# Optimization experiments

Measured on AMD Instinct MI355X. Metric: run time of the kernel, lower is better.

Reference implementation:

```python
import jax, jax.numpy as jnp
import numpy as np

B, T, W, R, N = 32, 256, 128, 4, 128
IFACE = R * W + 3 * W + 5 * R + 3   # 919
INSZ = (R + 1) * W                  # 640
DELTA = 1e-6

def _lstm_step(x, h, c, Wih, Whh, bih, bhh):
    g = x @ Wih.T + bih + h @ Whh.T + bhh
    i, f, gg, o = jnp.split(g, 4, axis=-1)
    c = jax.nn.sigmoid(f) * c + jax.nn.sigmoid(i) * jnp.tanh(gg)
    return jax.nn.sigmoid(o) * jnp.tanh(c), c

def _cosine(mem, keys):
    # mem [b,n,w], keys [b,h,w] -> [b,h,n]
    mn = mem / (jnp.linalg.norm(mem, axis=2, keepdims=True) + DELTA)
    kn = keys / (jnp.linalg.norm(keys, axis=2, keepdims=True) + DELTA)
    return jnp.einsum('bhw,bnw->bhn', kn, mn)

def _memory_step(xi, st):
    # xi: [b, IFACE] interface vector; st: DNC memory state
    mem, link, prec, rw, ww, usage = st
    b = xi.shape[0]
    o1 = R * W; o2 = o1 + R; o3 = o2 + W; o4 = o3 + 1
    o5 = o4 + W; o6 = o5 + W; o7 = o6 + R; o8 = o7 + 1; o9 = o8 + 1
    read_keys = jnp.tanh(xi[:, :o1].reshape(b, R, W))
    read_str = jax.nn.softplus(xi[:, o1:o2])
    write_key = jnp.tanh(xi[:, o2:o3])
    write_str = jax.nn.softplus(xi[:, o3:o4])
    erase = jax.nn.sigmoid(xi[:, o4:o5])
    write_vec = jnp.tanh(xi[:, o5:o6])
    free_gates = jax.nn.sigmoid(xi[:, o6:o7])
    alloc_gate = jax.nn.sigmoid(xi[:, o7:o8])
    write_gate = jax.nn.sigmoid(xi[:, o8:o9])
    read_modes = jax.nn.softmax(xi[:, o9:].reshape(b, R, 3), axis=-1)
    # usage vector update (single write head)
    usage = usage + (1 - usage) * ww
    usage = usage * jnp.prod(1 - free_gates[:, :, None] * rw, axis=1)
    # write content weighting [b,n]
    wc = jax.nn.softmax(_cosine(mem, write_key[:, None, :])[:, 0, :] * write_str, axis=1)
    # allocation weighting: sort ascending, exclusive cumprod, unsort
    u = DELTA + (1 - DELTA) * usage
    phi = jnp.argsort(u, axis=1)
    su = jnp.take_along_axis(u, phi, axis=1)
    prod_su = jnp.cumprod(jnp.concatenate([jnp.ones((b, 1), u.dtype), su], axis=1), axis=1)[:, :-1]
    alloc = jnp.take_along_axis((1 - su) * prod_su, jnp.argsort(phi, axis=1), axis=1)
    # write weighting [b,n]
    ww = write_gate * (alloc_gate * alloc + (1 - alloc_gate) * wc)
    # erase then write
    mem = mem * (1 - ww[:, :, None] * erase[:, None, :]) + ww[:, :, None] * write_vec[:, None, :]
    # temporal link matrix [b,n,n], zero diagonal
    link = (1 - ww[:, :, None] - ww[:, None, :]) * link + ww[:, :, None] * prec[:, None, :]
    link = link * (1 - jnp.eye(N, dtype=link.dtype))
    prec = (1 - jnp.sum(ww, axis=1, keepdims=True)) * prec + ww
    # read weighting: content + forward/backward temporal modes
    rc = jax.nn.softmax(_cosine(mem, read_keys) * read_str[:, :, None], axis=2)
    fw = jnp.einsum('bij,brj->bri', link, rw)
    bw = jnp.einsum('brj,bji->bri', rw, link)
    rw = read_modes[:, :, 0:1] * bw + read_modes[:, :, 1:2] * fw + read_modes[:, :, 2:3] * rc
    read_vecs = jnp.einsum('brn,bnw->bwr', rw, mem)  # [b,w,r] as used by controller
    return read_vecs, (mem, link, prec, rw, ww, usage)

def _forward(input, enc_Wih, enc_Whh, enc_bih, enc_bhh, ctl_Wih, ctl_Whh, ctl_bih, ctl_bhh, iface_W, iface_b, out_W, out_b):
    dt = input.dtype
    h0 = jnp.zeros((B, W), dt)
    def enc_step(carry, x_t):
        h, c = _lstm_step(x_t, carry[0], carry[1], enc_Wih, enc_Whh, enc_bih, enc_bhh)
        return (h, c), h
    _, enc = jax.lax.scan(enc_step, (h0, h0), jnp.swapaxes(input, 0, 1))  # enc: [T,B,W]
    z = lambda *s: jnp.zeros(s, dt)
    mem0 = (z(B, N, W), z(B, N, N), z(B, N), z(B, R, N), z(B, N), z(B, N))
    def step(carry, enc_t):
        h, c, rv, mst = carry
        # cat([b,w,1],[b,w,r]) then flatten -> interleaved per memory-cell element, as in torch
        x = jnp.concatenate([enc_t[:, :, None], rv], axis=2).reshape(B, INSZ)
        h, c = _lstm_step(x, h, c, ctl_Wih, ctl_Whh, ctl_bih, ctl_bhh)
        xi = h @ iface_W.T + iface_b
        rv, mst = _memory_step(xi, mst)
        out_t = jnp.concatenate([h, rv.reshape(B, W * R)], axis=1) @ out_W.T + out_b
        return (h, c, rv, mst), out_t
    _, outs = jax.lax.scan(step, (h0, h0, z(B, W, R), mem0), enc)
    return jnp.swapaxes(outs, 0, 1)  # [B,T,W]

def setup_inputs():
    key = jax.random.key(0)
    ks = jax.random.split(key, 8)
    p = lambda k, s: jax.random.normal(k, s, jnp.float32) * 0.05
    return {
        'input': jax.random.normal(ks[0], (B, T, W), jnp.float32),
        'source_lengths': jnp.full((B,), T, jnp.int32),
        'enc_Wih': p(ks[1], (4 * W, W)), 'enc_Whh': p(ks[2], (4 * W, W)),
        'enc_bih': jnp.zeros((4 * W,), jnp.float32), 'enc_bhh': jnp.zeros((4 * W,), jnp.float32),
        'ctl_Wih': p(ks[3], (4 * W, INSZ)), 'ctl_Whh': p(ks[4], (4 * W, W)),
        'ctl_bih': jnp.zeros((4 * W,), jnp.float32), 'ctl_bhh': jnp.zeros((4 * W,), jnp.float32),
        'iface_W': p(ks[5], (IFACE, W)), 'iface_b': jnp.zeros((IFACE,), jnp.float32),
        'out_W': p(ks[6], (W, INSZ)), 'out_b': jnp.zeros((W,), jnp.float32),
    }

def reference(input, source_lengths, enc_Wih, enc_Whh, enc_bih, enc_bhh, ctl_Wih, ctl_Whh, ctl_bih, ctl_bhh, iface_W, iface_b, out_W, out_b):
    # source_lengths are all == T (full-length sequences), so pack/pad is identity.
    return _forward(input, enc_Wih, enc_Whh, enc_bih, enc_bhh, ctl_Wih, ctl_Whh, ctl_bih, ctl_bhh, iface_W, iface_b, out_W, out_b)
```

## Files before the change

kernel.cpp:

```cpp
#include <hip/hip_runtime.h>

typedef unsigned short u16;
typedef unsigned int u32;

#define NT 1024
#define Bv 32
#define Tv 256
#define Wv 128
#define Rv 4
#define Nv 128
#define DELTAv 1e-6f

__device__ __forceinline__ float bf2f(u16 u){
  union { u32 i; float f; } c; c.i = ((u32)u) << 16; return c.f;
}
__device__ __forceinline__ u16 f2bf(float f){
  union { float f; u32 u; } c; c.f = f;
  u32 u = c.u;
  return (u16)((u + 0x7fffu + ((u >> 16) & 1u)) >> 16);
}
__device__ __forceinline__ void unp(u32 v, float& a, float& b){
  union { u32 i; float f; } c0, c1;
  c0.i = v << 16; c1.i = v & 0xffff0000u;
  a = c0.f; b = c1.f;
}
__device__ __forceinline__ float sigm(float x){ return 1.0f / (1.0f + __expf(-x)); }
__device__ __forceinline__ float softplusf(float x){ return fmaxf(x, 0.f) + log1pf(__expf(-fabsf(x))); }
__device__ __forceinline__ float wredsum(float v){
  #pragma unroll
  for (int o = 32; o > 0; o >>= 1) v += __shfl_down(v, o, 64);
  return v;
}
__device__ __forceinline__ float wredmax(float v){
  #pragma unroll
  for (int o = 32; o > 0; o >>= 1) v = fmaxf(v, __shfl_down(v, o, 64));
  return v;
}
__device__ __forceinline__ float ldval(const void* p, int idx, int dt32){
  return dt32 ? ((const float*)p)[idx] : bf2f(((const u16*)p)[idx]);
}
__device__ __forceinline__ float rl(float v, int l){
  union { int i; float f; } c;
  c.i = __builtin_amdgcn_readlane(__float_as_int(v), l);
  return c.f;
}

template<int ITERS, int STRIDE>
__device__ __forceinline__ float gemv_bf(const u32* __restrict__ wp, const float* __restrict__ xp){
  float a0 = 0.f, a1 = 0.f;
  u32 wb[8];
  #pragma unroll
  for (int i = 0; i < 8; i++) wb[i] = wp[i * STRIDE];
  #pragma unroll 1
  for (int c = 0; c < ITERS - 8; c += 8){
    u32 wn[8];
    #pragma unroll
    for (int i = 0; i < 8; i++) wn[i] = wp[(c + 8 + i) * STRIDE];
    #pragma unroll
    for (int i = 0; i < 8; i++){
      float w0, w1; unp(wb[i], w0, w1);
      float2 x2 = *(const float2*)(xp + 2 * (c + i));
      a0 = fmaf(x2.x, w0, a0); a1 = fmaf(x2.y, w1, a1);
      wb[i] = wn[i];
    }
  }
  #pragma unroll
  for (int i = 0; i < 8; i++){
    float w0, w1; unp(wb[i], w0, w1);
    float2 x2 = *(const float2*)(xp + 2 * (ITERS - 8 + i));
    a0 = fmaf(x2.x, w0, a0); a1 = fmaf(x2.y, w1, a1);
  }
  return a0 + a1;
}

template<int ITERS, int STRIDE>
__device__ __forceinline__ void gemv2_bf(const u32* __restrict__ wp0, const u32* __restrict__ wp1,
                                         const float* __restrict__ xp, float& r0, float& r1){
  float a0 = 0.f, a1 = 0.f, b0 = 0.f, b1 = 0.f;
  u32 wa[4], wb[4];
  #pragma unroll
  for (int i = 0; i < 4; i++){ wa[i] = wp0[i * STRIDE]; wb[i] = wp1[i * STRIDE]; }
  #pragma unroll 1
  for (int c = 0; c < ITERS - 4; c += 4){
    u32 na[4], nb[4];
    #pragma unroll
    for (int i = 0; i < 4; i++){ na[i] = wp0[(c + 4 + i) * STRIDE]; nb[i] = wp1[(c + 4 + i) * STRIDE]; }
    #pragma unroll
    for (int i = 0; i < 4; i++){
      float2 x2 = *(const float2*)(xp + 2 * (c + i));
      float w0, w1;
      unp(wa[i], w0, w1);
      a0 = fmaf(x2.x, w0, a0); a1 = fmaf(x2.y, w1, a1);
      unp(wb[i], w0, w1);
      b0 = fmaf(x2.x, w0, b0); b1 = fmaf(x2.y, w1, b1);
      wa[i] = na[i]; wb[i] = nb[i];
    }
  }
  #pragma unroll
  for (int i = 0; i < 4; i++){
    float2 x2 = *(const float2*)(xp + 2 * (ITERS - 4 + i));
    float w0, w1;
    unp(wa[i], w0, w1);
    a0 = fmaf(x2.x, w0, a0); a1 = fmaf(x2.y, w1, a1);
    unp(wb[i], w0, w1);
    b0 = fmaf(x2.x, w0, b0); b1 = fmaf(x2.y, w1, b1);
  }
  r0 = a0 + a1; r1 = b0 + b1;
}

__global__ void detect_dtype(const u16* __restrict__ buf, int* __restrict__ flag){
  int lane = threadIdx.x;
  float crazy = 0.f;
  for (int i = 0; i < 4; i++){
    u16 v = buf[lane * 4 + i];
    int e = (v >> 7) & 0xFF;
    if (e != 0 && (e < 117 || e > 137)) crazy += 1.f;
  }
  crazy = wredsum(crazy);
  if (lane == 0) flag[0] = (crazy >= 32.f) ? 1 : 0;
}

__device__ __forceinline__ u16 rdbf(const void* s, size_t idx, int f32){
  return f32 ? f2bf(((const float*)s)[idx]) : ((const u16*)s)[idx];
}

__global__ void pack_w(const void* __restrict__ src, u32* __restrict__ dst,
                       int Js, int Jd, int K, const int* __restrict__ flag){
  int j = blockIdx.x * 256 + threadIdx.x;
  int k2 = blockIdx.y;
  if (j >= Jd) return;
  u16 lo = 0, hi = 0;
  if (j < Js){
    lo = rdbf(src, (size_t)j * K + 2 * k2, flag[0]);
    hi = rdbf(src, (size_t)j * K + 2 * k2 + 1, flag[0]);
  }
  dst[(size_t)k2 * Jd + j] = (u32)lo | ((u32)hi << 16);
}

__device__ __forceinline__ int permctl(int c){
  if (c < 128) return 5 * c;
  int q = c - 128; return 5 * (q & 127) + 1 + (q >> 7);
}
__device__ __forceinline__ int permout(int c){
  if (c < 128) return c;
  int q = c - 128; return 128 + 4 * (q & 127) + (q >> 7);
}

__global__ void pack_ctl(const void* __restrict__ src, u32* __restrict__ dst,
                         const int* __restrict__ flag){
  int j = blockIdx.x * 256 + threadIdx.x;
  int k2 = blockIdx.y;
  if (j >= 512) return;
  u16 lo = rdbf(src, (size_t)j * 640 + permctl(2 * k2), flag[0]);
  u16 hi = rdbf(src, (size_t)j * 640 + permctl(2 * k2 + 1), flag[0]);
  dst[(size_t)k2 * 512 + j] = (u32)lo | ((u32)hi << 16);
}

__global__ void pack_out(const void* __restrict__ src, u32* __restrict__ dst,
                         const int* __restrict__ flag){
  int j = threadIdx.x;
  int k2 = blockIdx.y;
  if (j >= 128) return;
  u16 lo = rdbf(src, (size_t)j * 640 + permout(2 * k2), flag[0]);
  u16 hi = rdbf(src, (size_t)j * 640 + permout(2 * k2 + 1), flag[0]);
  dst[(size_t)k2 * 128 + j] = (u32)lo | ((u32)hi << 16);
}

__global__ void fill_half(u16* __restrict__ p, int n){
  int i = blockIdx.x * 256 + threadIdx.x;
  if (i < n) p[i] = 0x3F00;
}

__global__ __launch_bounds__(NT) void dnc_main(
    const void* __restrict__ input,
    const void* __restrict__ enc_bih_g, const void* __restrict__ enc_bhh_g,
    const void* __restrict__ ctl_bih_g, const void* __restrict__ ctl_bhh_g,
    const void* __restrict__ iface_b_g, const void* __restrict__ out_b_g,
    const u32* __restrict__ encPW, const u32* __restrict__ ctlPW,
    const u32* __restrict__ ifPW, const u32* __restrict__ outPW,
    void* __restrict__ outp, const int* __restrict__ dtflag)
{
  const int bid = blockIdx.x;
  const int tid = threadIdx.x;
  const int lane = tid & 63;
  const int wid = tid >> 6;
  const int dt32 = dtflag[0];

  __shared__ __align__(16) float memS[Nv * 129];
  __shared__ __align__(16) float linkS[Nv * 129];
  __shared__ __align__(16) float pp[NT];
  __shared__ __align__(16) float ppE[NT];
  __shared__ __align__(16) float xhC[768];
  __shared__ __align__(16) float xin2[2][128];
  __shared__ __align__(16) float rkeyS[512], rwS[512], rcS[512];
  __shared__ __align__(16) float wkeyS[128], eraseS[128], wvecS[128];
  __shared__ __align__(16) float wwS[128], usageS[128], precS[128], wcS[128];
  __shared__ __align__(16) float uS[128], sortedU[128], scanA[128], alS[128], sqS[128];
  __shared__ __align__(16) float encBias[512], ctlBias[512];
  __shared__ __align__(16) float outBias[128];
  __shared__ float rstrS[4], fgS[4], rmRaw[12], rmS[12], scal[8];

  float cE = 0.f;
  float cC = 0.f;

  if (tid < 512){
    encBias[tid] = ldval(enc_bih_g, tid, dt32) + ldval(enc_bhh_g, tid, dt32);
    ctlBias[tid] = ldval(ctl_bih_g, tid, dt32) + ldval(ctl_bhh_g, tid, dt32);
    rwS[tid] = 0.f;
  }
  if (tid < 768) xhC[tid] = 0.f;
  if (tid < 128){
    outBias[tid] = ldval(out_b_g, tid, dt32);
    wwS[tid] = 0.f; usageS[tid] = 0.f; precS[tid] = 0.f;
  }
  for (int i = tid; i < Nv * 129; i += NT){ memS[i] = 0.f; linkS[i] = 0.f; }
  if (tid < 64){
    int idx = (bid * Tv + 0) * Wv + 2 * tid;
    xin2[0][2 * tid] = ldval(input, idx, dt32);
    xin2[0][2 * tid + 1] = ldval(input, idx + 1, dt32);
  } else if (tid >= 64 && tid < 128){
    int w2 = (tid - 64) * 2;
    int idx = (bid * Tv + 1) * Wv + w2;
    xin2[1][w2] = ldval(input, idx, dt32);
    xin2[1][w2 + 1] = ldval(input, idx + 1, dt32);
  }
  __syncthreads();

  if (tid >= 512 && tid < 768){
    int o = tid - 512;
    float r0, r1;
    gemv2_bf<64, 512>(encPW + o, encPW + o + 256, xin2[0], r0, r1);
    rcS[o] = r0; rcS[o + 256] = r1;
  }
  __syncthreads();
  if (tid >= 896){
    int w = tid - 896;
    float g0 = rcS[w] + encBias[w];
    float g1 = rcS[128 + w] + encBias[128 + w];
    float g2 = rcS[256 + w] + encBias[256 + w];
    float g3 = rcS[384 + w] + encBias[384 + w];
    float cn = sigm(g1) * cE + sigm(g0) * tanhf(g2);
    cE = cn;
    xhC[w] = sigm(g3) * tanhf(cn);
  }
  __syncthreads();

  for (int t = 0; t < Tv; ++t){
    if (tid < 512){
      int s = tid >> 8, o = tid & 255;
      float r0, r1;
      gemv2_bf<192, 512>(ctlPW + (s * 192) * 512 + o, ctlPW + (s * 192) * 512 + o + 256,
                         xhC + s * 384, r0, r1);
      pp[s * 512 + o] = r0;
      pp[s * 512 + o + 256] = r1;
    } else if (tid < 768){
      int o = tid - 512;
      float r0, r1;
      gemv2_bf<64, 512>(encPW + o, encPW + o + 256, xin2[(t + 1) & 1], r0, r1);
      rcS[o] = r0; rcS[o + 256] = r1;
    } else if (tid < 896){
      if (t > 0){
        int w = tid - 768;
        float o = outBias[w];
        #pragma unroll
        for (int s = 0; s < 8; s++) o += ppE[s * 128 + w];
        size_t oi = ((size_t)bid * Tv + (t - 1)) * Wv + w;
        if (dt32) ((float*)outp)[oi] = o;
        else ((u16*)outp)[oi] = f2bf(o);
      }
    } else if (tid >= 960){
      int w2 = (tid - 960) * 2;
      int col = (t + 2 < Tv) ? t + 2 : Tv - 1;
      int idx = (bid * Tv + col) * Wv + w2;
      xin2[t & 1][w2] = ldval(input, idx, dt32);
      xin2[t & 1][w2 + 1] = ldval(input, idx + 1, dt32);
    }
    __syncthreads();

    if (tid < 128){
      float g0 = pp[tid] + pp[512 + tid] + ctlBias[tid];
      float g1 = pp[128 + tid] + pp[640 + tid] + ctlBias[128 + tid];
      float g2 = pp[256 + tid] + pp[768 + tid] + ctlBias[256 + tid];
      float g3 = pp[384 + tid] + pp[896 + tid] + ctlBias[384 + tid];
      float cn = sigm(g1) * cC + sigm(g0) * tanhf(g2);
      cC = cn;
      xhC[640 + tid] = sigm(g3) * tanhf(cn);
    } else if (tid >= 512 && tid < 768){
      int o = tid - 512;
      float r0, r1;
      gemv2_bf<64, 512>(encPW + 64 * 512 + o, encPW + 64 * 512 + o + 256, xhC, r0, r1);
      ppE[o] = rcS[o] + r0;
      ppE[o + 256] = rcS[o + 256] + r1;
    }
    __syncthreads();

    if (tid < 464){
      float r0, r1;
      gemv2_bf<64, 928>(ifPW + tid, ifPW + tid + 464, xhC + 640, r0, r1);
      pp[tid] = r0 + ldval(iface_b_g, tid, dt32);
      pp[tid + 464] = r1 + ((tid + 464 < 919) ? ldval(iface_b_g, tid + 464, dt32) : 0.f);
    } else if (tid >= 896){
      int w = tid - 896;
      float g0 = ppE[w] + encBias[w];
      float g1 = ppE[128 + w] + encBias[128 + w];
      float g2 = ppE[256 + w] + encBias[256 + w];
      float g3 = ppE[384 + w] + encBias[384 + w];
      float cn = sigm(g1) * cE + sigm(g0) * tanhf(g2);
      cE = cn;
      xhC[w] = sigm(g3) * tanhf(cn);
    }
    __syncthreads();

    if (tid < 919){
      float v = pp[tid];
      if (tid < 512) rkeyS[tid] = tanhf(v);
      else if (tid < 516) rstrS[tid - 512] = softplusf(v);
      else if (tid < 644) wkeyS[tid - 516] = tanhf(v);
      else if (tid == 644) scal[0] = softplusf(v);
      else if (tid < 773) eraseS[tid - 645] = sigm(v);
      else if (tid < 901) wvecS[tid - 773] = tanhf(v);
      else if (tid < 905) fgS[tid - 901] = sigm(v);
      else if (tid == 905) scal[1] = sigm(v);
      else if (tid == 906) scal[2] = sigm(v);
      else rmRaw[tid - 907] = v;
    }
    __syncthreads();

    if (wid < 5){
      float* arr = (wid < 4) ? (rkeyS + wid * 128) : wkeyS;
      float a = arr[lane], bq = arr[lane + 64];
      float s = wredsum(a * a + bq * bq);
      s = __shfl(s, 0, 64);
      float inv = 1.0f / (sqrtf(s) + DELTAv);
      arr[lane] = a * inv; arr[lane + 64] = bq * inv;
    } else if (wid < 7){
      int n = (wid - 5) * 64 + lane;
      float us = usageS[n];
      us = us + (1.f - us) * wwS[n];
      float ret = (1.f - fgS[0] * rwS[n]) * (1.f - fgS[1] * rwS[128 + n]) *
                  (1.f - fgS[2] * rwS[256 + n]) * (1.f - fgS[3] * rwS[384 + n]);
      us *= ret;
      usageS[n] = us;
      uS[n] = DELTAv + (1.f - DELTAv) * us;
    } else if (tid >= 448 && tid < 452){
      int r = tid - 448;
      float m0 = rmRaw[3 * r], m1 = rmRaw[3 * r + 1], m2 = rmRaw[3 * r + 2];
      float mx = fmaxf(m0, fmaxf(m1, m2));
      float e0 = __expf(m0 - mx), e1 = __expf(m1 - mx), e2 = __expf(m2 - mx);
      float s = e0 + e1 + e2;
      rmS[3 * r] = e0 / s; rmS[3 * r + 1] = e1 / s; rmS[3 * r + 2] = e2 / s;
    } else if (wid >= 8 && wid < 10){
      int n = (wid - 8) * 64 + lane;
      float sq = 0.f;
      #pragma unroll 8
      for (int j = 0; j < 128; j++){
        float m = memS[n * 129 + j];
        sq = fmaf(m, m, sq);
      }
      sqS[n] = sq;
    }
    __syncthreads();

    if (tid < 128){
      float wk0 = wkeyS[lane], wk1 = wkeyS[64 + lane];
      float dt = 0.f;
      #pragma unroll 128
      for (int j = 0; j < 128; j++){
        float m = memS[tid * 129 + j];
        dt = fmaf(rl((j < 64) ? wk0 : wk1, j & 63), m, dt);
      }
      wcS[tid] = dt / (sqrtf(sqS[tid]) + DELTAv) * scal[0];
    }
    __syncthreads();

    if (wid == 0){
      float a = wcS[lane], bq = wcS[lane + 64];
      float mx = wredmax(fmaxf(a, bq)); mx = __shfl(mx, 0, 64);
      float ea = __expf(a - mx), eb = __expf(bq - mx);
      float s = wredsum(ea + eb); s = __shfl(s, 0, 64);
      wcS[lane] = ea / s; wcS[lane + 64] = eb / s;
    } else if (wid == 1){
      int l = lane;
      float u0 = uS[l], u1 = uS[64 + l];
      int r0 = 0, r1 = 0;
      for (int m = 0; m < 128; m++){
        float um = uS[m];
        r0 += (um < u0) || (um == u0 && m < l);
        r1 += (um < u1) || (um == u1 && m < 64 + l);
      }
      sortedU[r0] = u0; sortedU[r1] = u1;
      float a = sortedU[2 * l], bq = sortedU[2 * l + 1];
      float p = a * bq;
      float incl = p;
      #pragma unroll
      for (int o = 1; o < 64; o <<= 1){
        float tv = __shfl_up(incl, o, 64);
        if (l >= o) incl *= tv;
      }
      float exh = __shfl_up(incl, 1, 64);
      if (l == 0) exh = 1.f;
      scanA[2 * l] = exh;
      scanA[2 * l + 1] = exh * a;
      float ex0 = scanA[r0], ex1 = scanA[r1];
      alS[l] = (1.f - u0) * ex0;
      alS[64 + l] = (1.f - u1) * ex1;
    }
    __syncthreads();

    if (wid == 0){
      float w0v = scal[2] * (scal[1] * alS[lane] + (1.f - scal[1]) * wcS[lane]);
      float w1v = scal[2] * (scal[1] * alS[64 + lane] + (1.f - scal[1]) * wcS[64 + lane]);
      wwS[lane] = w0v; wwS[64 + lane] = w1v;
      float s = wredsum(w0v + w1v);
      if (lane == 0) scal[3] = s;
    }
    __syncthreads();

    #pragma unroll
    for (int it = 0; it < 16; it++){
      int e = it * NT + tid;
      int n = e >> 7, w = e & 127;
      float wwn = wwS[n];
      float m = memS[n * 129 + w];
      memS[n * 129 + w] = m * (1.f - wwn * eraseS[w]) + wwn * wvecS[w];
      float l = linkS[n * 129 + w];
      linkS[n * 129 + w] = (n == w) ? 0.f
        : ((1.f - wwn - wwS[w]) * l + wwn * precS[w]);
    }
    __syncthreads();

    if (tid < 128){
      int i = tid;
      float rwreg[8];
      #pragma unroll
      for (int q = 0; q < 8; q++) rwreg[q] = rwS[q * 64 + lane];
      float f0 = 0.f, f1 = 0.f, f2 = 0.f, f3 = 0.f;
      float b0 = 0.f, b1 = 0.f, b2 = 0.f, b3 = 0.f;
      #pragma unroll 128
      for (int j = 0; j < 128; j++){
        float lr = linkS[i * 129 + j];
        float lc = linkS[j * 129 + i];
        float w0 = rl(rwreg[j >> 6], j & 63);
        float w1 = rl(rwreg[2 + (j >> 6)], j & 63);
        float w2 = rl(rwreg[4 + (j >> 6)], j & 63);
        float w3 = rl(rwreg[6 + (j >> 6)], j & 63);
        f0 = fmaf(w0, lr, f0); b0 = fmaf(w0, lc, b0);
        f1 = fmaf(w1, lr, f1); b1 = fmaf(w1, lc, b1);
        f2 = fmaf(w2, lr, f2); b2 = fmaf(w2, lc, b2);
        f3 = fmaf(w3, lr, f3); b3 = fmaf(w3, lc, b3);
      }
      pp[i] = f0; pp[128 + i] = f1; pp[256 + i] = f2; pp[384 + i] = f3;
      pp[512 + i] = b0; pp[640 + i] = b1; pp[768 + i] = b2; pp[896 + i] = b3;
    } else if (tid < 256){
      int n = tid - 128;
      float kreg[8];
      #pragma unroll
      for (int q = 0; q < 8; q++) kreg[q] = rkeyS[q * 64 + lane];
      float sq = 0.f, d0 = 0.f, d1 = 0.f, d2 = 0.f, d3 = 0.f;
      #pragma unroll 128
      for (int j = 0; j < 128; j++){
        float m = memS[n * 129 + j];
        sq = fmaf(m, m, sq);
        d0 = fmaf(rl(kreg[j >> 6], j & 63), m, d0);
        d1 = fmaf(rl(kreg[2 + (j >> 6)], j & 63), m, d1);
        d2 = fmaf(rl(kreg[4 + (j >> 6)], j & 63), m, d2);
        d3 = fmaf(rl(kreg[6 + (j >> 6)], j & 63), m, d3);
      }
      float inv = 1.f / (sqrtf(sq) + DELTAv);
      rcS[n]       = d0 * inv * rstrS[0];
      rcS[128 + n] = d1 * inv * rstrS[1];
      rcS[256 + n] = d2 * inv * rstrS[2];
      rcS[384 + n] = d3 * inv * rstrS[3];
    } else if (tid < 384){
      int n = tid - 256;
      precS[n] = (1.f - scal[3]) * precS[n] + wwS[n];
    }
    __syncthreads();

    if (wid < 4){
      int r = wid;
      float a = rcS[r * 128 + lane], bq = rcS[r * 128 + 64 + lane];
      float mx = wredmax(fmaxf(a, bq)); mx = __shfl(mx, 0, 64);
      float ea = __expf(a - mx), eb = __expf(bq - mx);
      float s = wredsum(ea + eb); s = __shfl(s, 0, 64);
      float pa = ea / s, pb = eb / s;
      int o0 = r * 128 + lane, o1 = o0 + 64;
      rwS[o0] = rmS[3 * r] * pp[512 + o0] + rmS[3 * r + 1] * pp[o0] + rmS[3 * r + 2] * pa;
      rwS[o1] = rmS[3 * r] * pp[512 + o1] + rmS[3 * r + 1] * pp[o1] + rmS[3 * r + 2] * pb;
    }
    __syncthreads();

    if (tid < 128){
      int w = tid;
      float rwreg[8];
      #pragma unroll
      for (int q = 0; q < 8; q++) rwreg[q] = rwS[q * 64 + lane];
      float a0 = 0.f, a1 = 0.f, a2 = 0.f, a3 = 0.f;
      #pragma unroll 128
      for (int n = 0; n < 128; n++){
        float m = memS[n * 129 + w];
        a0 = fmaf(rl(rwreg[n >> 6], n & 63), m, a0);
        a1 = fmaf(rl(rwreg[2 + (n >> 6)], n & 63), m, a1);
        a2 = fmaf(rl(rwreg[4 + (n >> 6)], n & 63), m, a2);
        a3 = fmaf(rl(rwreg[6 + (n >> 6)], n & 63), m, a3);
      }
      xhC[128 + w] = a0;
      xhC[256 + w] = a1;
      xhC[384 + w] = a2;
      xhC[512 + w] = a3;
    } else if (tid >= 512){
      int s = (tid - 512) >> 7, j = tid & 127;
      ppE[tid] = gemv_bf<16, 128>(outPW + (s * 16) * 128 + j, xhC + 640 + 32 * s);
    }
    __syncthreads();

    if (tid < 512){
      int s = tid >> 7, j = tid & 127;
      ppE[tid] = gemv_bf<64, 128>(outPW + (64 + s * 64) * 128 + j, xhC + 128 + 128 * s);
    }
    __syncthreads();
  }

  if (tid < 128){
    float o = outBias[tid];
    #pragma unroll
    for (int s = 0; s < 8; s++) o += ppE[s * 128 + tid];
    size_t oi = ((size_t)bid * Tv + (Tv - 1)) * Wv + tid;
    if (dt32) ((float*)outp)[oi] = o;
    else ((u16*)outp)[oi] = f2bf(o);
  }
}

extern "C" void kernel_launch(void* const* d_in, const int* in_sizes, int n_in,
                              void* d_out, int out_size, void* d_ws, size_t ws_size,
                              hipStream_t stream) {
  (void)in_sizes; (void)n_in;
  const void* input   = d_in[0];
  const void* enc_Wih = d_in[2];
  const void* enc_Whh = d_in[3];
  const void* enc_bih = d_in[4];
  const void* enc_bhh = d_in[5];
  const void* ctl_Wih = d_in[6];
  const void* ctl_Whh = d_in[7];
  const void* ctl_bih = d_in[8];
  const void* ctl_bhh = d_in[9];
  const void* iface_W = d_in[10];
  const void* iface_b = d_in[11];
  const void* out_W   = d_in[12];
  const void* out_b   = d_in[13];

  char* ws = (char*)d_ws;
  size_t off = 0;
  int* dtflag = (int*)(ws + off); off += 256;
  u32* encPW = (u32*)(ws + off); off += (size_t)128 * 512 * 4;
  u32* ctlPW = (u32*)(ws + off); off += (size_t)384 * 512 * 4;
  u32* ifPW  = (u32*)(ws + off); off += (size_t)64 * 928 * 4;
  u32* outPW = (u32*)(ws + off); off += (size_t)320 * 128 * 4;
  const size_t need_bytes = off;

  if (ws_size < need_bytes){
    fill_half<<<dim3((out_size + 255) / 256), dim3(256), 0, stream>>>((u16*)d_out, out_size);
    return;
  }

  detect_dtype<<<dim3(1), dim3(64), 0, stream>>>((const u16*)input, dtflag);

  pack_w<<<dim3(2, 64), 256, 0, stream>>>(enc_Wih, encPW, 512, 512, 128, dtflag);
  pack_w<<<dim3(2, 64), 256, 0, stream>>>(enc_Whh, encPW + 64 * 512, 512, 512, 128, dtflag);
  pack_ctl<<<dim3(2, 320), 256, 0, stream>>>(ctl_Wih, ctlPW, dtflag);
  pack_w<<<dim3(2, 64), 256, 0, stream>>>(ctl_Whh, ctlPW + 320 * 512, 512, 512, 128, dtflag);
  pack_w<<<dim3(4, 64), 256, 0, stream>>>(iface_W, ifPW, 919, 928, 128, dtflag);
  pack_out<<<dim3(1, 320), 128, 0, stream>>>(out_W, outPW, dtflag);

  dnc_main<<<dim3(Bv), dim3(NT), 0, stream>>>(
      input, enc_bih, enc_bhh, ctl_bih, ctl_bhh, iface_b, out_b,
      encPW, ctlPW, ifPW, outPW, d_out, dtflag);
}
```

Measured before the change: 10.89 ms.

## Rebalance per-step DNC phases across threads and remove two barriers

Reorganizes the per-timestep schedule of the persistent single-block DNC kernel. The write-key content dot products and memory row norms are split across more threads in halves, and key normalization is folded into scalar factors. The read-key and link gemvs are spread over two thread groups each. The read-vector output projection is deferred into the next step's first phase, which removes two __syncthreads per step. The intent is to shorten the serial critical path of each recurrent step, at the cost of more partial-sum traffic through shared memory and reshuffled buffer reuse (rcS/ppE), which adds ordering risk.

```diff
diff --git a/kernel.cpp b/kernel.cpp
--- a/kernel.cpp
+++ b/kernel.cpp
@@ -198,7 +198,7 @@
   __shared__ __align__(16) float uS[128], sortedU[128], scanA[128], alS[128], sqS[128];
   __shared__ __align__(16) float encBias[512], ctlBias[512];
   __shared__ __align__(16) float outBias[128];
-  __shared__ float rstrS[4], fgS[4], rmRaw[12], rmS[12], scal[8];
+  __shared__ float rstrS[4], fgS[4], rmRaw[12], rmS[12], scal[16];
 
   float cE = 0.f;
   float cC = 0.f;
@@ -258,22 +258,10 @@
       float r0, r1;
       gemv2_bf<64, 512>(encPW + o, encPW + o + 256, xin2[(t + 1) & 1], r0, r1);
       rcS[o] = r0; rcS[o + 256] = r1;
-    } else if (tid < 896){
-      if (t > 0){
-        int w = tid - 768;
-        float o = outBias[w];
-        #pragma unroll
-        for (int s = 0; s < 8; s++) o += ppE[s * 128 + w];
-        size_t oi = ((size_t)bid * Tv + (t - 1)) * Wv + w;
-        if (dt32) ((float*)outp)[oi] = o;
-        else ((u16*)outp)[oi] = f2bf(o);
-      }
-    } else if (tid >= 960){
-      int w2 = (tid - 960) * 2;
-      int col = (t + 2 < Tv) ? t + 2 : Tv - 1;
-      int idx = (bid * Tv + col) * Wv + w2;
-      xin2[t & 1][w2] = ldval(input, idx, dt32);
-      xin2[t & 1][w2 + 1] = ldval(input, idx + 1, dt32);
+    } else {
+      int q = tid - 768;
+      int s = q >> 7, j = q & 127;
+      ppE[q] = gemv_bf<128, 128>(outPW + (64 + s * 128) * 128 + j, xhC + 128 + 256 * s);
     }
     __syncthreads();
 
@@ -285,12 +273,27 @@
       float cn = sigm(g1) * cC + sigm(g0) * tanhf(g2);
       cC = cn;
       xhC[640 + tid] = sigm(g3) * tanhf(cn);
+    } else if (tid < 256){
+      if (t > 0){
+        int w = tid - 128;
+        float o = outBias[w] + ppE[w] + ppE[128 + w]
+                + ppE[512 + w] + ppE[640 + w] + ppE[768 + w] + ppE[896 + w];
+        size_t oi = ((size_t)bid * Tv + (t - 1)) * Wv + w;
+        if (dt32) ((float*)outp)[oi] = o;
+        else ((u16*)outp)[oi] = f2bf(o);
+      }
     } else if (tid >= 512 && tid < 768){
       int o = tid - 512;
       float r0, r1;
       gemv2_bf<64, 512>(encPW + 64 * 512 + o, encPW + 64 * 512 + o + 256, xhC, r0, r1);
-      ppE[o] = rcS[o] + r0;
-      ppE[o + 256] = rcS[o + 256] + r1;
+      rcS[o] = rcS[o] + r0;
+      rcS[o + 256] = rcS[o + 256] + r1;
+    } else if (tid >= 768 && tid < 832){
+      int w2 = (tid - 768) * 2;
+      int col = (t + 2 < Tv) ? t + 2 : Tv - 1;
+      int idx = (bid * Tv + col) * Wv + w2;
+      xin2[t & 1][w2] = ldval(input, idx, dt32);
+      xin2[t & 1][w2 + 1] = ldval(input, idx + 1, dt32);
     }
     __syncthreads();
 
@@ -301,10 +304,10 @@
       pp[tid + 464] = r1 + ((tid + 464 < 919) ? ldval(iface_b_g, tid + 464, dt32) : 0.f);
     } else if (tid >= 896){
       int w = tid - 896;
-      float g0 = ppE[w] + encBias[w];
-      float g1 = ppE[128 + w] + encBias[128 + w];
-      float g2 = ppE[256 + w] + encBias[256 + w];
-      float g3 = ppE[384 + w] + encBias[384 + w];
+      float g0 = rcS[w] + encBias[w];
+      float g1 = rcS[128 + w] + encBias[128 + w];
+      float g2 = rcS[256 + w] + encBias[256 + w];
+      float g3 = rcS[384 + w] + encBias[384 + w];
       float cn = sigm(g1) * cE + sigm(g0) * tanhf(g2);
       cE = cn;
       xhC[w] = sigm(g3) * tanhf(cn);
@@ -326,15 +329,25 @@
     }
     __syncthreads();
 
-    if (wid < 5){
-      float* arr = (wid < 4) ? (rkeyS + wid * 128) : wkeyS;
-      float a = arr[lane], bq = arr[lane + 64];
-      float s = wredsum(a * a + bq * bq);
-      s = __shfl(s, 0, 64);
-      float inv = 1.0f / (sqrtf(s) + DELTAv);
-      arr[lane] = a * inv; arr[lane + 64] = bq * inv;
-    } else if (wid < 7){
-      int n = (wid - 5) * 64 + lane;
+    if (tid < 256){
+      int n = tid & 127, hf = tid >> 7;
+      float wk = wkeyS[hf * 64 + lane];
+      const float* mrow = memS + n * 129 + hf * 64;
+      float dt = 0.f;
+      #pragma unroll 64
+      for (int jj = 0; jj < 64; jj++) dt = fmaf(rl(wk, jj), mrow[jj], dt);
+      pp[tid] = dt;
+    } else if (tid < 512){
+      int r = wid - 4;
+      float a = rkeyS[r * 128 + lane], b = rkeyS[r * 128 + 64 + lane];
+      float s = wredsum(a * a + b * b);
+      if (lane == 0) scal[4 + r] = 1.f / (sqrtf(s) + DELTAv);
+    } else if (tid < 576){
+      float a = wkeyS[lane], b = wkeyS[64 + lane];
+      float s = wredsum(a * a + b * b);
+      if (lane == 0) scal[8] = 1.f / (sqrtf(s) + DELTAv);
+    } else if (tid < 704){
+      int n = tid - 576;
       float us = usageS[n];
       us = us + (1.f - us) * wwS[n];
       float ret = (1.f - fgS[0] * rwS[n]) * (1.f - fgS[1] * rwS[128 + n]) *
@@ -342,39 +355,32 @@
       us *= ret;
       usageS[n] = us;
       uS[n] = DELTAv + (1.f - DELTAv) * us;
-    } else if (tid >= 448 && tid < 452){
-      int r = tid - 448;
+    } else if (tid < 960){
+      int q = tid - 704;
+      int n = q & 127, hf = q >> 7;
+      const float* mrow = memS + n * 129 + hf * 64;
+      float sq = 0.f;
+      #pragma unroll 64
+      for (int jj = 0; jj < 64; jj++){ float m = mrow[jj]; sq = fmaf(m, m, sq); }
+      pp[tid] = sq;
+    } else if (tid < 964){
+      int r = tid - 960;
       float m0 = rmRaw[3 * r], m1 = rmRaw[3 * r + 1], m2 = rmRaw[3 * r + 2];
       float mx = fmaxf(m0, fmaxf(m1, m2));
       float e0 = __expf(m0 - mx), e1 = __expf(m1 - mx), e2 = __expf(m2 - mx);
       float s = e0 + e1 + e2;
       rmS[3 * r] = e0 / s; rmS[3 * r + 1] = e1 / s; rmS[3 * r + 2] = e2 / s;
-    } else if (wid >= 8 && wid < 10){
-      int n = (wid - 8) * 64 + lane;
-      float sq = 0.f;
-      #pragma unroll 8
-      for (int j = 0; j < 128; j++){
-        float m = memS[n * 129 + j];
-        sq = fmaf(m, m, sq);
-      }
-      sqS[n] = sq;
-    }
-    __syncthreads();
-
-    if (tid < 128){
-      float wk0 = wkeyS[lane], wk1 = wkeyS[64 + lane];
-      float dt = 0.f;
-      #pragma unroll 128
-      for (int j = 0; j < 128; j++){
-        float m = memS[tid * 129 + j];
-        dt = fmaf(rl((j < 64) ? wk0 : wk1, j & 63), m, dt);
-      }
-      wcS[tid] = dt / (sqrtf(sqS[tid]) + DELTAv) * scal[0];
     }
     __syncthreads();
 
     if (wid == 0){
-      float a = wcS[lane], bq = wcS[lane + 64];
+      float d0 = pp[lane] + pp[128 + lane];
+      float d1 = pp[64 + lane] + pp[192 + lane];
+      float q0 = pp[704 + lane] + pp[832 + lane];
+      float q1 = pp[768 + lane] + pp[896 + lane];
+      float kfac = scal[8] * scal[0];
+      float a  = d0 / (sqrtf(q0) + DELTAv) * kfac;
+      float bq = d1 / (sqrtf(q1) + DELTAv) * kfac;
       float mx = wredmax(fmaxf(a, bq)); mx = __shfl(mx, 0, 64);
       float ea = __expf(a - mx), eb = __expf(bq - mx);
       float s = wredsum(ea + eb); s = __shfl(s, 0, 64);
@@ -429,57 +435,53 @@
     }
     __syncthreads();
 
-    if (tid < 128){
-      int i = tid;
-      float rwreg[8];
-      #pragma unroll
-      for (int q = 0; q < 8; q++) rwreg[q] = rwS[q * 64 + lane];
-      float f0 = 0.f, f1 = 0.f, f2 = 0.f, f3 = 0.f;
-      float b0 = 0.f, b1 = 0.f, b2 = 0.f, b3 = 0.f;
+    if (tid < 256){
+      int i = tid & 127, rg = tid >> 7;
+      int rA = 2 * rg, rB = rA + 1;
+      float rwA0 = rwS[rA * 128 + lane], rwA1 = rwS[rA * 128 + 64 + lane];
+      float rwB0 = rwS[rB * 128 + lane], rwB1 = rwS[rB * 128 + 64 + lane];
+      float fA = 0.f, fB = 0.f, bA = 0.f, bB = 0.f;
       #pragma unroll 128
       for (int j = 0; j < 128; j++){
         float lr = linkS[i * 129 + j];
         float lc = linkS[j * 129 + i];
-        float w0 = rl(rwreg[j >> 6], j & 63);
-        float w1 = rl(rwreg[2 + (j >> 6)], j & 63);
-        float w2 = rl(rwreg[4 + (j >> 6)], j & 63);
-        float w3 = rl(rwreg[6 + (j >> 6)], j & 63);
-        f0 = fmaf(w0, lr, f0); b0 = fmaf(w0, lc, b0);
-        f1 = fmaf(w1, lr, f1); b1 = fmaf(w1, lc, b1);
-        f2 = fmaf(w2, lr, f2); b2 = fmaf(w2, lc, b2);
-        f3 = fmaf(w3, lr, f3); b3 = fmaf(w3, lc, b3);
+        float wA = rl((j < 64) ? rwA0 : rwA1, j & 63);
+        float wB = rl((j < 64) ? rwB0 : rwB1, j & 63);
+        fA = fmaf(wA, lr, fA); bA = fmaf(wA, lc, bA);
+        fB = fmaf(wB, lr, fB); bB = fmaf(wB, lc, bB);
       }
-      pp[i] = f0; pp[128 + i] = f1; pp[256 + i] = f2; pp[384 + i] = f3;
-      pp[512 + i] = b0; pp[640 + i] = b1; pp[768 + i] = b2; pp[896 + i] = b3;
-    } else if (tid < 256){
-      int n = tid - 128;
-      float kreg[8];
-      #pragma unroll
-      for (int q = 0; q < 8; q++) kreg[q] = rkeyS[q * 64 + lane];
-      float sq = 0.f, d0 = 0.f, d1 = 0.f, d2 = 0.f, d3 = 0.f;
+      pp[rA * 128 + i] = fA; pp[rB * 128 + i] = fB;
+      pp[512 + rA * 128 + i] = bA; pp[512 + rB * 128 + i] = bB;
+    } else if (tid < 512){
+      int q = tid - 256;
+      int n = q & 127, rg = q >> 7;
+      int rA = 2 * rg, rB = rA + 1;
+      float kA0 = rkeyS[rA * 128 + lane], kA1 = rkeyS[rA * 128 + 64 + lane];
+      float kB0 = rkeyS[rB * 128 + lane], kB1 = rkeyS[rB * 128 + 64 + lane];
+      float sq = 0.f, dA = 0.f, dB = 0.f;
       #pragma unroll 128
       for (int j = 0; j < 128; j++){
         float m = memS[n * 129 + j];
-        sq = fmaf(m, m, sq);
-        d0 = fmaf(rl(kreg[j >> 6], j & 63), m, d0);
-        d1 = fmaf(rl(kreg[2 + (j >> 6)], j & 63), m, d1);
-        d2 = fmaf(rl(kreg[4 + (j >> 6)], j & 63), m, d2);
-        d3 = fmaf(rl(kreg[6 + (j >> 6)], j & 63), m, d3);
+        if (rg == 0) sq = fmaf(m, m, sq);
+        dA = fmaf(rl((j < 64) ? kA0 : kA1, j & 63), m, dA);
+        dB = fmaf(rl((j < 64) ? kB0 : kB1, j & 63), m, dB);
       }
-      float inv = 1.f / (sqrtf(sq) + DELTAv);
-      rcS[n]       = d0 * inv * rstrS[0];
-      rcS[128 + n] = d1 * inv * rstrS[1];
-      rcS[256 + n] = d2 * inv * rstrS[2];
-      rcS[384 + n] = d3 * inv * rstrS[3];
-    } else if (tid < 384){
-      int n = tid - 256;
-      precS[n] = (1.f - scal[3]) * precS[n] + wwS[n];
+      rcS[rA * 128 + n] = dA;
+      rcS[rB * 128 + n] = dB;
+      if (rg == 0) sqS[n] = sq;
+    } else {
+      int s = (tid - 512) >> 7, j = tid & 127;
+      ppE[tid] = gemv_bf<16, 128>(outPW + (s * 16) * 128 + j, xhC + 640 + 32 * s);
     }
     __syncthreads();
 
     if (wid < 4){
       int r = wid;
-      float a = rcS[r * 128 + lane], bq = rcS[r * 128 + 64 + lane];
+      float fac = scal[4 + r] * rstrS[r];
+      float im0 = 1.f / (sqrtf(sqS[lane]) + DELTAv);
+      float im1 = 1.f / (sqrtf(sqS[64 + lane]) + DELTAv);
+      float a  = rcS[r * 128 + lane] * im0 * fac;
+      float bq = rcS[r * 128 + 64 + lane] * im1 * fac;
       float mx = wredmax(fmaxf(a, bq)); mx = __shfl(mx, 0, 64);
       float ea = __expf(a - mx), eb = __expf(bq - mx);
       float s = wredsum(ea + eb); s = __shfl(s, 0, 64);
@@ -487,44 +489,32 @@
       int o0 = r * 128 + lane, o1 = o0 + 64;
       rwS[o0] = rmS[3 * r] * pp[512 + o0] + rmS[3 * r + 1] * pp[o0] + rmS[3 * r + 2] * pa;
       rwS[o1] = rmS[3 * r] * pp[512 + o1] + rmS[3 * r + 1] * pp[o1] + rmS[3 * r + 2] * pb;
-    }
-    __syncthreads();
-
-    if (tid < 128){
-      int w = tid;
-      float rwreg[8];
-      #pragma unroll
-      for (int q = 0; q < 8; q++) rwreg[q] = rwS[q * 64 + lane];
-      float a0 = 0.f, a1 = 0.f, a2 = 0.f, a3 = 0.f;
+    } else if (tid >= 256 && tid < 384){
+      int n = tid - 256;
+      precS[n] = (1.f - scal[3]) * precS[n] + wwS[n];
+    }
+    __syncthreads();
+
+    if (tid < 512){
+      int r = tid >> 7, w = tid & 127;
+      float rw0 = rwS[r * 128 + lane], rw1 = rwS[r * 128 + 64 + lane];
+      float acc = 0.f;
       #pragma unroll 128
-      for (int n = 0; n < 128; n++){
-        float m = memS[n * 129 + w];
-        a0 = fmaf(rl(rwreg[n >> 6], n & 63), m, a0);
-        a1 = fmaf(rl(rwreg[2 + (n >> 6)], n & 63), m, a1);
-        a2 = fmaf(rl(rwreg[4 + (n >> 6)], n & 63), m, a2);
-        a3 = fmaf(rl(rwreg[6 + (n >> 6)], n & 63), m, a3);
-      }
-      xhC[128 + w] = a0;
-      xhC[256 + w] = a1;
-      xhC[384 + w] = a2;
-      xhC[512 + w] = a3;
-    } else if (tid >= 512){
-      int s = (tid - 512) >> 7, j = tid & 127;
-      ppE[tid] = gemv_bf<16, 128>(outPW + (s * 16) * 128 + j, xhC + 640 + 32 * s);
-    }
-    __syncthreads();
-
-    if (tid < 512){
-      int s = tid >> 7, j = tid & 127;
-      ppE[tid] = gemv_bf<64, 128>(outPW + (64 + s * 64) * 128 + j, xhC + 128 + 128 * s);
-    }
-    __syncthreads();
-  }
-
+      for (int n = 0; n < 128; n++)
+        acc = fmaf(rl((n < 64) ? rw0 : rw1, n & 63), memS[n * 129 + w], acc);
+      xhC[128 + tid] = acc;
+    }
+    __syncthreads();
+  }
+
+  if (tid < 256){
+    int s = tid >> 7, j = tid & 127;
+    ppE[tid] = gemv_bf<128, 128>(outPW + (64 + s * 128) * 128 + j, xhC + 128 + 256 * s);
+  }
+  __syncthreads();
   if (tid < 128){
-    float o = outBias[tid];
-    #pragma unroll
-    for (int s = 0; s < 8; s++) o += ppE[s * 128 + tid];
+    float o = outBias[tid] + ppE[tid] + ppE[128 + tid]
+            + ppE[512 + tid] + ppE[640 + tid] + ppE[768 + tid] + ppE[896 + tid];
     size_t oi = ((size_t)bid * Tv + (Tv - 1)) * Wv + tid;
     if (dt32) ((float*)outp)[oi] = o;
     else ((u16*)outp)[oi] = f2bf(o);
```

Result: faster. 9.014 ms, median of 2 (-17.2%).
